# Optimization experiments

Hardware: AMD Instinct MI355X
Metric: run time of the kernel (lower is better)

The kernel has to match this reference:

```python
import jax, jax.numpy as jnp
import numpy as np
from jax import lax

# Fixed dims from MSSMamba defaults
B_, L_, DM = 2, 8192, 256
NH, HP, NS = 4, 64, 8          # nheads, headdim, d_state
DIN = NH * HP                  # d_inner = 256
DPROJ = 2 * DIN + 2 * NS + NH  # 532


def setup_inputs() -> dict:
    key = jax.random.key(0)
    ks = jax.random.split(key, 16)
    f = lambda k, s, sc=1.0: jax.random.normal(k, s, jnp.float32) * sc
    inp = {
        'x_H': f(ks[0], (B_, L_, DM)),
        'x_V': f(ks[1], (B_, L_, DM)),
        'W_in_H': f(ks[2], (DM, 2 * DPROJ), 0.05),
        'W_in_V': f(ks[3], (DM, 2 * DPROJ), 0.05),
        'W_out_HF': f(ks[4], (DIN, DM), 0.05),
        'W_out_HB': f(ks[5], (DIN, DM), 0.05),
        'W_out_VF': f(ks[6], (DIN, DM), 0.05),
        'W_out_VB': f(ks[7], (DIN, DM), 0.05),
        'W_out': f(ks[8], (4 * DM, DM), 0.05),
    }
    for i, nm in enumerate(['HF', 'HB', 'VF', 'VB']):
        kd = jax.random.fold_in(ks[9], i)
        ka = jax.random.fold_in(ks[10], i)
        inp['dt_bias_' + nm] = f(kd, (NH,), 0.1)
        inp['A_log_' + nm] = jnp.log(jax.random.uniform(ka, (NH,), jnp.float32, 1.0, 16.0))
        inp['D_' + nm] = jnp.ones((NH,), jnp.float32)
    # per-batch permutation mapping vertical position -> horizontal position
    inp['v2h'] = jax.vmap(lambda k: jax.random.permutation(k, L_))(
        jax.random.split(ks[11], B_)).astype(jnp.int32)
    return inp


def _scan_dir(zxbcdt, dt_bias, A_log, D):
    # zxbcdt: [b, l, DPROJ] -> Mamba2-style selective scan, ngroups=1
    z = zxbcdt[..., :DIN].reshape(B_, L_, NH, HP)
    xBC = jax.nn.silu(zxbcdt[..., DIN:DIN + DIN + 2 * NS])
    x = xBC[..., :DIN].reshape(B_, L_, NH, HP)
    Bm = xBC[..., DIN:DIN + NS]      # [b, l, n]
    Cm = xBC[..., DIN + NS:]         # [b, l, n]
    dt = jax.nn.softplus(zxbcdt[..., -NH:] + dt_bias)  # [b, l, h]
    A = -jnp.exp(A_log)              # [h]
    dA = jnp.exp(dt * A)             # [b, l, h]
    dBx = jnp.einsum('blh,bln,blhp->blhpn', dt, Bm, x)  # [b,l,h,p,n]

    def step(state, inp):
        dA_t, dBx_t, C_t = inp
        state = dA_t[..., None, None] * state + dBx_t   # [b,h,p,n]
        y_t = jnp.einsum('bhpn,bn->bhp', state, C_t)
        return state, y_t

    init = jnp.zeros((B_, NH, HP, NS), dt.dtype)
    _, ys = lax.scan(step, init, (jnp.moveaxis(dA, 1, 0),
                                  jnp.moveaxis(dBx, 1, 0),
                                  jnp.moveaxis(Cm, 1, 0)))
    y = jnp.moveaxis(ys, 0, 1) + D[None, None, :, None] * x  # skip D*x
    y = y * jax.nn.silu(z)                                   # gate
    return y.reshape(B_, L_, DIN)


def reference(x_H, x_V, W_in_H, W_in_V,
              dt_bias_HF, dt_bias_HB, dt_bias_VF, dt_bias_VB,
              A_log_HF, A_log_HB, A_log_VF, A_log_VB,
              D_HF, D_HB, D_VF, D_VB,
              W_out_HF, W_out_HB, W_out_VF, W_out_VB,
              W_out, v2h):
    zx_HF, zx_HB = jnp.split(x_H @ W_in_H, 2, axis=-1)
    zx_VF, zx_VB = jnp.split(x_V @ W_in_V, 2, axis=-1)
    # note: source applies out_proj_HB to the HF branch (kept faithful)
    y_HF = _scan_dir(zx_HF, dt_bias_HF, A_log_HF, D_HF) @ W_out_HB
    y_HB = _scan_dir(zx_HB[:, ::-1], dt_bias_HB, A_log_HB, D_HB)[:, ::-1] @ W_out_HF
    y_VF = _scan_dir(zx_VF, dt_bias_VF, A_log_VF, D_VF) @ W_out_VB
    y_VB = _scan_dir(zx_VB[:, ::-1], dt_bias_VB, A_log_VB, D_VB)[:, ::-1] @ W_out_VF
    # remap vertical-ordered outputs to horizontal ordering (scatter by v2h)
    bidx = jnp.arange(B_)[:, None]
    y_VF = jnp.zeros_like(y_VF).at[bidx, v2h].set(y_VF)
    y_VB = jnp.zeros_like(y_VB).at[bidx, v2h].set(y_VB)
    cat = jnp.concatenate([y_HF, y_HB, y_VF, y_VB], axis=-1)  # [b, l, 4*d_model]
    return jax.nn.silu(cat) @ W_out
```

## Files before the change

### kernel.cpp

```cpp
#include <hip/hip_runtime.h>
#include <hip/hip_bf16.h>

#define B_N 2
#define L_N 8192
#define ROWS 16384
#define CHUNK 64
#define NCHUNK 128
#define GRP 16
#define NGRP 8
#define NPAD 1152

typedef __bf16 bf16x8 __attribute__((ext_vector_type(8)));
typedef float f32x4 __attribute__((ext_vector_type(4)));

__device__ __forceinline__ float siluf(float v) {
  return v * __builtin_amdgcn_rcpf(1.f + __expf(-v));
}
__device__ __forceinline__ float softplusf_(float v) {
  return fmaxf(v, 0.f) + log1pf(__expf(-fabsf(v)));
}
__device__ __forceinline__ unsigned short f2bf(float v) {
  union { __bf16 b; unsigned short u; } x;
  x.b = (__bf16)v;
  return x.u;
}
__device__ __forceinline__ float bf2f(unsigned short u) {
  union { unsigned u; float f; } x; x.u = ((unsigned)u) << 16;
  return x.f;
}

__device__ __forceinline__ void gload_lds16(const unsigned short* g, unsigned short* l) {
  __builtin_amdgcn_global_load_lds(
      (const __attribute__((address_space(1))) unsigned int*)g,
      (__attribute__((address_space(3))) unsigned int*)l, 16, 0, 0);
}

struct P4 { const float* p[4]; };
struct ScanConsts {
  const float* dt_bias[4];
  const float* A_log[4];
  const float* D[4];
};

__global__ __launch_bounds__(256) void k_prep(
    const float* __restrict__ xH, const float* __restrict__ xV,
    const float* __restrict__ WH, const float* __restrict__ WV,
    P4 ws, const float* __restrict__ W_out, const int* __restrict__ v2h, ScanConsts sc,
    unsigned short* __restrict__ xbf, float* __restrict__ dtv_arr, float* __restrict__ dA_arr,
    unsigned short* __restrict__ Wt_in, unsigned short* __restrict__ Wt_dirs,
    unsigned short* __restrict__ Wt_fin, int* __restrict__ inv) {
  __shared__ float xs[32][257];
  __shared__ float Wsm[8][260];
  int bid = blockIdx.x;
  int tid = threadIdx.x;
  if (bid < 1024) {
    const int mat = bid >> 9;
    const float* x = mat ? xV : xH;
    const float* W = mat ? WV : WH;
    const int r0 = (bid & 511) * 32;
    for (int i = tid; i < 2048; i += 256) {
      int c = i >> 8, k = i & 255;
      int sl = c >> 2, h = c & 3;
      Wsm[c][k] = W[(long)k * 1064 + sl * 532 + 528 + h];
    }
    for (int i = tid; i < 32 * 64; i += 256) {
      int rl = i >> 6, kq = (i & 63) * 4;
      float4 v = *(const float4*)(x + (long)(r0 + rl) * 256 + kq);
      xs[rl][kq + 0] = v.x; xs[rl][kq + 1] = v.y; xs[rl][kq + 2] = v.z; xs[rl][kq + 3] = v.w;
    }
    __syncthreads();
    for (int i = tid; i < 32 * 64; i += 256) {
      int rl = i >> 6, kq = (i & 63) * 4;
      ushort4 o;
      o.x = f2bf(xs[rl][kq + 0]);
      o.y = f2bf(xs[rl][kq + 1]);
      o.z = f2bf(xs[rl][kq + 2]);
      o.w = f2bf(xs[rl][kq + 3]);
      *(ushort4*)(xbf + (size_t)mat * ROWS * 256 + (long)(r0 + rl) * 256 + kq) = o;
    }
    const int rl = tid >> 3, c = tid & 7;
    float s = 0.f;
    #pragma unroll 8
    for (int k = 0; k < 256; ++k) s = fmaf(xs[rl][k], Wsm[c][k], s);
    const int sl = c >> 2, h = c & 3;
    const int dir = mat * 2 + sl;
    float dtv = softplusf_(s + sc.dt_bias[dir][h]);
    float dAv = __expf(dtv * (-__expf(sc.A_log[dir][h])));
    long o = ((long)dir * 4 + h) * ROWS + (r0 + rl);
    dtv_arr[o] = dtv;
    dA_arr[o] = dAv;
  } else if (bid < 3328) {
    int i = (bid - 1024) * 256 + tid;
    int z = i / (NPAD * 256);
    int rem = i - z * (NPAD * 256);
    int n = rem >> 8, k = rem & 255;
    const float* W = z ? WV : WH;
    int sl = n >= 544;
    int cc = n - (sl ? 544 : 0);
    float v = (cc < 532) ? W[(long)k * 1064 + sl * 532 + cc] : 0.f;
    Wt_in[i] = f2bf(v);
  } else if (bid < 4352) {
    int i = (bid - 3328) * 256 + tid;
    int d = i >> 16;
    int rem = i & 65535;
    int n = rem >> 8, k = rem & 255;
    Wt_dirs[i] = f2bf(ws.p[d][(long)k * 256 + n]);
  } else if (bid < 5376) {
    int i = (bid - 4352) * 256 + tid;
    int n = i >> 10, k = i & 1023;
    Wt_fin[i] = f2bf(W_out[(long)k * 256 + n]);
  } else {
    int m = (bid - 5376) * 256 + tid;
    if (m < ROWS) {
      int b = m >> 13;
      inv[b * L_N + v2h[m]] = m;
    }
  }
}

struct EpiIn {
  unsigned short* zraw;
  unsigned short* xraw;
  unsigned short* bc;
};

__global__ __launch_bounds__(256) void k_gemm_in(
    const unsigned short* __restrict__ Abase, const unsigned short* __restrict__ Btbase,
    EpiIn ep) {
  __shared__ unsigned short smem[24576];
  const int tid = threadIdx.x;
  const int lane = tid & 63;
  const int wid = tid >> 6;
  const int wm = wid & 1, wn = wid >> 1;
  const int q = lane >> 4, r = lane & 15;
  const int hbid = blockIdx.x;
  const int xcd = hbid & 7;
  const int j = hbid >> 3;
  const int m0 = (xcd * 16 + (j & 15)) * 128;
  const int n0 = ((j >> 4) % 9) * 128;
  const int z = j / 144;
  const unsigned short* A = Abase + (long)z * ROWS * 256;
  const unsigned short* Bt = Btbase + (long)z * NPAD * 256;

  int s_row[2], s_ch[2];
  #pragma unroll
  for (int i = 0; i < 2; ++i) {
    int idx = i * 256 + tid;
    s_row[i] = idx >> 2;
    s_ch[i] = (idx & 3) ^ ((s_row[i] >> 1) & 3);
  }

  auto stage = [&](int ti) {
    const int slot = ti % 3;
    const int kt = ti * 32;
    #pragma unroll
    for (int i = 0; i < 2; ++i) {
      gload_lds16(A + (long)(m0 + s_row[i]) * 256 + kt + s_ch[i] * 8,
                  smem + (size_t)slot * 4096 + (size_t)(i * 256 + wid * 64) * 8);
      gload_lds16(Bt + (long)(n0 + s_row[i]) * 256 + kt + s_ch[i] * 8,
                  smem + 12288 + (size_t)slot * 4096 + (size_t)(i * 256 + wid * 64) * 8);
    }
  };

  f32x4 acc[4][4] = {};
  const int swr = (r >> 1) & 3;

  stage(0);
  stage(1);

  #pragma unroll
  for (int i = 0; i < 8; ++i) {
    if (i < 7) asm volatile("s_waitcnt vmcnt(4)" ::: "memory");
    else       asm volatile("s_waitcnt vmcnt(0)" ::: "memory");
    __builtin_amdgcn_s_barrier();
    __builtin_amdgcn_sched_barrier(0);
    if (i + 2 < 8) stage(i + 2);
    const int slot = i % 3;
    bf16x8 af[4], bfr[4];
    #pragma unroll
    for (int mi = 0; mi < 4; ++mi)
      af[mi] = *(const bf16x8*)&smem[(size_t)slot * 4096 +
                                     ((wm * 64 + mi * 16 + r) * 4 + (q ^ swr)) * 8];
    #pragma unroll
    for (int ni = 0; ni < 4; ++ni)
      bfr[ni] = *(const bf16x8*)&smem[12288 + (size_t)slot * 4096 +
                                      ((wn * 64 + ni * 16 + r) * 4 + (q ^ swr)) * 8];
    __builtin_amdgcn_s_setprio(1);
    #pragma unroll
    for (int mi = 0; mi < 4; ++mi)
      #pragma unroll
      for (int ni = 0; ni < 4; ++ni)
        acc[mi][ni] = __builtin_amdgcn_mfma_f32_16x16x32_bf16(af[mi], bfr[ni], acc[mi][ni], 0, 0, 0);
    __builtin_amdgcn_s_setprio(0);
  }
  __syncthreads();

  unsigned short* tr = smem + wid * (16 * 72);
  #pragma unroll
  for (int mi = 0; mi < 4; ++mi) {
    #pragma unroll
    for (int ni = 0; ni < 4; ++ni)
      #pragma unroll
      for (int j2 = 0; j2 < 4; ++j2)
        tr[(q * 4 + j2) * 72 + ni * 16 + r] = f2bf(acc[mi][ni][j2]);
    asm volatile("s_waitcnt lgkmcnt(0)" ::: "memory");
    #pragma unroll
    for (int pass = 0; pass < 2; ++pass) {
      int rl = pass * 8 + (lane >> 3);
      int c8 = (lane & 7) * 8;
      bf16x8 v = *(const bf16x8*)&tr[rl * 72 + c8];
      int row = m0 + wm * 64 + mi * 16 + rl;
      int col = n0 + wn * 64 + c8;
      int sl = col >= 544;
      int cc = col - (sl ? 544 : 0);
      if (cc < 528) {
        int dir = z * 2 + sl;
        if (cc < 256)
          *(bf16x8*)(ep.zraw + ((long)dir * ROWS + row) * 256 + cc) = v;
        else if (cc < 512)
          *(bf16x8*)(ep.xraw + ((long)dir * ROWS + row) * 256 + cc - 256) = v;
        else
          *(bf16x8*)(ep.bc + ((long)dir * ROWS + row) * 16 + cc - 512) = v;
      }
    }
    asm volatile("s_waitcnt lgkmcnt(0)" ::: "memory");
  }
}

__global__ __launch_bounds__(512) void k_fuse(
    const unsigned short* __restrict__ ybf,
    const unsigned short* __restrict__ Wt_dirs,
    const unsigned short* __restrict__ Wt_fin,
    const int* __restrict__ inv,
    float* __restrict__ out) {
  __shared__ unsigned short smf[47616];
  unsigned short* Ab = smf;
  unsigned short* Bb = smf + 6144;
  unsigned short* Tl = smf + 30720;
  float* Ttmp = (float*)(smf + 30720);
  const int tid = threadIdx.x;
  const int lane = tid & 63;
  const int wid = tid >> 6;
  const int wm = wid & 1, wn = wid >> 1;
  const int q = lane >> 4, r = lane & 15;
  const int r0 = blockIdx.x * 64;
  const int swr = (r >> 1) & 3;

  const int a_row = tid >> 2;
  const int a_ch = (tid & 3) ^ ((a_row >> 1) & 3);
  const long a_offH = (long)(r0 + a_row) * 256 + a_ch * 8;
  long a_offV = 0;
  if (tid < 256) a_offV = (long)inv[r0 + a_row] * 256 + a_ch * 8;
  int b_row[2], b_ch[2];
  #pragma unroll
  for (int rnd = 0; rnd < 2; ++rnd) {
    int idx = rnd * 512 + tid;
    b_row[rnd] = idx >> 2;
    b_ch[rnd] = (idx & 3) ^ ((b_row[rnd] >> 1) & 3);
  }

  auto stageT = [&](int g) {
    const int seg = g >> 3, ti = g & 7, kt = ti * 32;
    const int dl = seg >> 1;
    const int slot = g % 3;
    if ((seg & 1) == 0) {
      const long aoff = (dl >= 2) ? a_offV : a_offH;
      if (tid < 256)
        gload_lds16(ybf + (long)dl * ROWS * 256 + aoff + kt,
                    Ab + (size_t)slot * 2048 + (size_t)(wid * 64) * 8);
      #pragma unroll
      for (int rnd = 0; rnd < 2; ++rnd)
        gload_lds16(Wt_dirs + (long)dl * 65536 + (long)b_row[rnd] * 256 + kt + b_ch[rnd] * 8,
                    Bb + (size_t)slot * 8192 + (size_t)(rnd * 512 + wid * 64) * 8);
    } else {
      #pragma unroll
      for (int rnd = 0; rnd < 2; ++rnd)
        gload_lds16(Wt_fin + (long)b_row[rnd] * 1024 + dl * 256 + kt + b_ch[rnd] * 8,
                    Bb + (size_t)slot * 8192 + (size_t)(rnd * 512 + wid * 64) * 8);
    }
  };

  f32x4 acc_o[2][4] = {};

  stageT(0);
  stageT(1);

  #pragma unroll
  for (int d = 0; d < 4; ++d) {
    f32x4 acc_t[2][4] = {};
    #pragma unroll
    for (int i = 0; i < 8; ++i) {
      const int g = d * 16 + i;
      asm volatile("s_waitcnt vmcnt(2)" ::: "memory");
      __builtin_amdgcn_s_barrier();
      __builtin_amdgcn_sched_barrier(0);
      stageT(g + 2);
      const int slot = g % 3;
      bf16x8 af[2], bfr[4];
      #pragma unroll
      for (int mi = 0; mi < 2; ++mi)
        af[mi] = *(const bf16x8*)&Ab[(size_t)slot * 2048 +
                                     ((wm * 32 + mi * 16 + r) * 4 + (q ^ swr)) * 8];
      #pragma unroll
      for (int ni = 0; ni < 4; ++ni)
        bfr[ni] = *(const bf16x8*)&Bb[(size_t)slot * 8192 +
                                      ((wn * 64 + ni * 16 + r) * 4 + (q ^ swr)) * 8];
      __builtin_amdgcn_s_setprio(1);
      #pragma unroll
      for (int mi = 0; mi < 2; ++mi)
        #pragma unroll
        for (int ni = 0; ni < 4; ++ni)
          acc_t[mi][ni] = __builtin_amdgcn_mfma_f32_16x16x32_bf16(af[mi], bfr[ni], acc_t[mi][ni], 0, 0, 0);
      __builtin_amdgcn_s_setprio(0);
    }
    #pragma unroll
    for (int mi = 0; mi < 2; ++mi)
      #pragma unroll
      for (int ni = 0; ni < 4; ++ni)
        #pragma unroll
        for (int jj = 0; jj < 4; ++jj)
          Tl[(wm * 32 + mi * 16 + q * 4 + jj) * 264 + wn * 64 + ni * 16 + r] =
              f2bf(siluf(acc_t[mi][ni][jj]));
    asm volatile("s_waitcnt lgkmcnt(0)" ::: "memory");
    #pragma unroll
    for (int i = 0; i < 8; ++i) {
      const int g = d * 16 + 8 + i;
      if (g < 63) asm volatile("s_waitcnt vmcnt(2)" ::: "memory");
      else        asm volatile("s_waitcnt vmcnt(0)" ::: "memory");
      __builtin_amdgcn_s_barrier();
      __builtin_amdgcn_sched_barrier(0);
      if (g + 2 < 64) stageT(g + 2);
      const int slot = g % 3;
      const int kt = i * 32;
      bf16x8 af[2], bfr[4];
      #pragma unroll
      for (int mi = 0; mi < 2; ++mi)
        af[mi] = *(const bf16x8*)&Tl[(wm * 32 + mi * 16 + r) * 264 + kt + q * 8];
      #pragma unroll
      for (int ni = 0; ni < 4; ++ni)
        bfr[ni] = *(const bf16x8*)&Bb[(size_t)slot * 8192 +
                                      ((wn * 64 + ni * 16 + r) * 4 + (q ^ swr)) * 8];
      __builtin_amdgcn_s_setprio(1);
      #pragma unroll
      for (int mi = 0; mi < 2; ++mi)
        #pragma unroll
        for (int ni = 0; ni < 4; ++ni)
          acc_o[mi][ni] = __builtin_amdgcn_mfma_f32_16x16x32_bf16(af[mi], bfr[ni], acc_o[mi][ni], 0, 0, 0);
      __builtin_amdgcn_s_setprio(0);
    }
  }

  __syncthreads();
  #pragma unroll
  for (int h = 0; h < 2; ++h) {
    if (wm == h) {
      #pragma unroll
      for (int mi = 0; mi < 2; ++mi)
        #pragma unroll
        for (int ni = 0; ni < 4; ++ni)
          #pragma unroll
          for (int jj = 0; jj < 4; ++jj)
            Ttmp[(mi * 16 + q * 4 + jj) * 260 + wn * 64 + ni * 16 + r] = acc_o[mi][ni][jj];
    }
    __syncthreads();
    #pragma unroll
    for (int pass = 0; pass < 4; ++pass) {
      int id = pass * 512 + tid;
      int row = id >> 6, c4 = (id & 63) * 4;
      float4 v = *(const float4*)&Ttmp[row * 260 + c4];
      *(float4*)(out + (long)(r0 + h * 32 + row) * 256 + c4) = v;
    }
    if (h == 0) __syncthreads();
  }
}

struct ScanP {
  const unsigned short* xraw;
  const unsigned short* zraw;
  const unsigned short* bc;
  const float* dtv;
  const float* dA;
  const float* D[4];
};

__global__ __launch_bounds__(512) void k_scan1(ScanP sp, float* __restrict__ S,
                                               float* __restrict__ P) {
  __shared__ __align__(16) float Bst[8][CHUNK][8];
  __shared__ float dAs[8][CHUNK];
  const int tid = threadIdx.x;
  const int p = tid & 63;
  const int w = tid >> 6;
  const int c = blockIdx.x;
  const int d = blockIdx.y;
  const int bh = w;
  const int b = bh >> 2, h = bh & 3;
  const int rev = d & 1;
  const int t0 = c * CHUNK;
  {
    const int t = t0 + p;
    const int l = rev ? (L_N - 1 - t) : t;
    const int row = (b << 13) + l;
    uint4 bv = *(const uint4*)(sp.bc + ((long)d * ROWS + row) * 16);
    const unsigned short* bu = (const unsigned short*)&bv;
    float dtvv = sp.dtv[((long)d * 4 + h) * ROWS + row];
    dAs[w][p] = sp.dA[((long)d * 4 + h) * ROWS + row];
    #pragma unroll
    for (int n = 0; n < 8; ++n) Bst[w][p][n] = siluf(bf2f(bu[n])) * dtvv;
  }
  __syncthreads();

  float st[8] = {0, 0, 0, 0, 0, 0, 0, 0};
  float cumdA = 1.f;
  const int l0 = rev ? (L_N - 1 - t0) : t0;
  const unsigned short* xp = sp.xraw + ((long)d * ROWS + (b << 13) + l0) * 256 + h * 64 + p;
  const long stp = rev ? -256L : 256L;

  unsigned short xa[4], xb[4];
  #pragma unroll
  for (int j = 0; j < 4; ++j) xa[j] = xp[(long)j * stp];
  #pragma unroll
  for (int g = 0; g < CHUNK / 4; ++g) {
    if (g < CHUNK / 4 - 1) {
      #pragma unroll
      for (int j = 0; j < 4; ++j) xb[j] = xp[(long)((g + 1) * 4 + j) * stp];
    }
    #pragma unroll
    for (int j = 0; j < 4; ++j) {
      int s = g * 4 + j;
      float x = siluf(bf2f(xa[j]));
      float dA = dAs[w][s];
      f32x4 B0 = *(const f32x4*)&Bst[w][s][0];
      f32x4 B1 = *(const f32x4*)&Bst[w][s][4];
      cumdA *= dA;
      st[0] = fmaf(dA, st[0], x * B0[0]);
      st[1] = fmaf(dA, st[1], x * B0[1]);
      st[2] = fmaf(dA, st[2], x * B0[2]);
      st[3] = fmaf(dA, st[3], x * B0[3]);
      st[4] = fmaf(dA, st[4], x * B1[0]);
      st[5] = fmaf(dA, st[5], x * B1[1]);
      st[6] = fmaf(dA, st[6], x * B1[2]);
      st[7] = fmaf(dA, st[7], x * B1[3]);
    }
    #pragma unroll
    for (int j = 0; j < 4; ++j) xa[j] = xb[j];
  }
  float* Sp = S + ((((long)d * NCHUNK + c) * 8 + bh) * 64 + p) * 8;
  #pragma unroll
  for (int n = 0; n < 8; ++n) Sp[n] = st[n];
  if (p == 0) P[((long)d * NCHUNK + c) * 8 + bh] = cumdA;
}

__global__ __launch_bounds__(512) void k_scan2a(const float* __restrict__ S,
                                                const float* __restrict__ P,
                                                float* __restrict__ carry_loc,
                                                float* __restrict__ Sg,
                                                float* __restrict__ Pg) {
  __shared__ float Pl[GRP];
  const int tid = threadIdx.x;
  const int gid = blockIdx.x;
  const int g = gid & (NGRP - 1);
  const int dbh = gid >> 3;
  const int d = dbh >> 3, bh = dbh & 7;
  if (tid < GRP) Pl[tid] = P[((long)d * NCHUNK + g * GRP + tid) * 8 + bh];
  __syncthreads();
  float cy = 0.f;
  #pragma unroll
  for (int i = 0; i < GRP; ++i) {
    const int c = g * GRP + i;
    carry_loc[(((long)d * NCHUNK + c) * 8 + bh) * 512 + tid] = cy;
    const float Sv = S[(((long)d * NCHUNK + c) * 8 + bh) * 512 + tid];
    cy = fmaf(Pl[i], cy, Sv);
  }
  Sg[(((long)d * NGRP + g) * 8 + bh) * 512 + tid] = cy;
  if (tid == 0) {
    float pp = 1.f;
    #pragma unroll
    for (int i = 0; i < GRP; ++i) pp *= Pl[i];
    Pg[((long)d * NGRP + g) * 8 + bh] = pp;
  }
}

__global__ __launch_bounds__(512) void k_scan2b(const float* __restrict__ Sg,
                                                const float* __restrict__ Pg,
                                                float* __restrict__ gcarry) {
  __shared__ float Pgl[NGRP];
  const int tid = threadIdx.x;
  const int dbh = blockIdx.x;
  const int d = dbh >> 3, bh = dbh & 7;
  if (tid < NGRP) Pgl[tid] = Pg[((long)d * NGRP + tid) * 8 + bh];
  __syncthreads();
  float cy = 0.f;
  #pragma unroll
  for (int g = 0; g < NGRP; ++g) {
    gcarry[(((long)d * NGRP + g) * 8 + bh) * 512 + tid] = cy;
    const float Sv = Sg[(((long)d * NGRP + g) * 8 + bh) * 512 + tid];
    cy = fmaf(Pgl[g], cy, Sv);
  }
}

__global__ __launch_bounds__(512) void k_scan3(ScanP sp,
                                               const float* __restrict__ carry_loc,
                                               const float* __restrict__ gcarry,
                                               const float* __restrict__ Pc,
                                               unsigned short* __restrict__ ybf) {
  __shared__ __align__(16) float Bst[8][CHUNK][8];
  __shared__ __align__(16) float Cst[8][CHUNK][8];
  __shared__ float dAs[8][CHUNK];
  __shared__ float Pgr[8][GRP];
  const int tid = threadIdx.x;
  const int p = tid & 63;
  const int w = tid >> 6;
  const int c = blockIdx.x;
  const int d = blockIdx.y;
  const int bh = w;
  const int b = bh >> 2, h = bh & 3;
  const int rev = d & 1;
  const float Dv = sp.D[d][h];
  const int t0 = c * CHUNK;
  const int grp = c >> 4, ii = c & 15;
  if (p < ii) Pgr[w][p] = Pc[((long)d * NCHUNK + grp * GRP + p) * 8 + bh];
  {
    const int t = t0 + p;
    const int l = rev ? (L_N - 1 - t) : t;
    const int row = (b << 13) + l;
    const unsigned short* bp = sp.bc + ((long)d * ROWS + row) * 16;
    uint4 bv = *(const uint4*)bp;
    uint4 cv = *(const uint4*)(bp + 8);
    const unsigned short* bu = (const unsigned short*)&bv;
    const unsigned short* cu = (const unsigned short*)&cv;
    float dtvv = sp.dtv[((long)d * 4 + h) * ROWS + row];
    dAs[w][p] = sp.dA[((long)d * 4 + h) * ROWS + row];
    #pragma unroll
    for (int n = 0; n < 8; ++n) Bst[w][p][n] = siluf(bf2f(bu[n])) * dtvv;
    #pragma unroll
    for (int n = 0; n < 8; ++n) Cst[w][p][n] = siluf(bf2f(cu[n]));
  }
  __syncthreads();

  float pref = 1.f;
  for (int k = 0; k < ii; ++k) pref *= Pgr[w][k];
  float st[8];
  {
    const float* clp = carry_loc + ((((long)d * NCHUNK + c) * 8 + bh) * 64 + p) * 8;
    const float* gcp = gcarry + ((((long)d * NGRP + grp) * 8 + bh) * 64 + p) * 8;
    #pragma unroll
    for (int n = 0; n < 8; ++n) st[n] = fmaf(pref, gcp[n], clp[n]);
  }

  const int l0 = rev ? (L_N - 1 - t0) : t0;
  const long base = (long)(b << 13) + l0;
  const unsigned short* xp = sp.xraw + ((long)d * ROWS + base) * 256 + h * 64 + p;
  const unsigned short* zp = sp.zraw + ((long)d * ROWS + base) * 256 + h * 64 + p;
  unsigned short* yp = ybf + ((long)d * ROWS + base) * 256 + h * 64 + p;
  const long stp = rev ? -256L : 256L;

  unsigned short xa[4], xb[4], za[4], zb[4];
  #pragma unroll
  for (int j = 0; j < 4; ++j) { xa[j] = xp[(long)j * stp]; za[j] = zp[(long)j * stp]; }
  #pragma unroll
  for (int g = 0; g < CHUNK / 4; ++g) {
    if (g < CHUNK / 4 - 1) {
      #pragma unroll
      for (int j = 0; j < 4; ++j) {
        xb[j] = xp[(long)((g + 1) * 4 + j) * stp];
        zb[j] = zp[(long)((g + 1) * 4 + j) * stp];
      }
    }
    #pragma unroll
    for (int j = 0; j < 4; ++j) {
      int s = g * 4 + j;
      float x = siluf(bf2f(xa[j]));
      float zv = siluf(bf2f(za[j]));
      float dA = dAs[w][s];
      f32x4 B0 = *(const f32x4*)&Bst[w][s][0];
      f32x4 B1 = *(const f32x4*)&Bst[w][s][4];
      f32x4 C0 = *(const f32x4*)&Cst[w][s][0];
      f32x4 C1 = *(const f32x4*)&Cst[w][s][4];
      st[0] = fmaf(dA, st[0], x * B0[0]);
      st[1] = fmaf(dA, st[1], x * B0[1]);
      st[2] = fmaf(dA, st[2], x * B0[2]);
      st[3] = fmaf(dA, st[3], x * B0[3]);
      st[4] = fmaf(dA, st[4], x * B1[0]);
      st[5] = fmaf(dA, st[5], x * B1[1]);
      st[6] = fmaf(dA, st[6], x * B1[2]);
      st[7] = fmaf(dA, st[7], x * B1[3]);
      float y01 = fmaf(st[1], C0[1], st[0] * C0[0]);
      float y23 = fmaf(st[3], C0[3], st[2] * C0[2]);
      float y45 = fmaf(st[5], C1[1], st[4] * C1[0]);
      float y67 = fmaf(st[7], C1[3], st[6] * C1[2]);
      float y = (y01 + y23) + (y45 + y67);
      y = fmaf(Dv, x, y) * zv;
      yp[(long)s * stp] = f2bf(y);
    }
    #pragma unroll
    for (int j = 0; j < 4; ++j) { xa[j] = xb[j]; za[j] = zb[j]; }
  }
}

extern "C" void kernel_launch(void* const* d_in, const int* in_sizes, int n_in,
                              void* d_out, int out_size, void* d_ws, size_t ws_size,
                              hipStream_t stream) {
  const float* x_H = (const float*)d_in[0];
  const float* x_V = (const float*)d_in[1];
  const float* W_in_H = (const float*)d_in[2];
  const float* W_in_V = (const float*)d_in[3];
  const float* W_out_HF = (const float*)d_in[4];
  const float* W_out_HB = (const float*)d_in[5];
  const float* W_out_VF = (const float*)d_in[6];
  const float* W_out_VB = (const float*)d_in[7];
  const float* W_out = (const float*)d_in[8];
  const float* dt_bias_HF = (const float*)d_in[9];
  const float* A_log_HF = (const float*)d_in[10];
  const float* D_HF = (const float*)d_in[11];
  const float* dt_bias_HB = (const float*)d_in[12];
  const float* A_log_HB = (const float*)d_in[13];
  const float* D_HB = (const float*)d_in[14];
  const float* dt_bias_VF = (const float*)d_in[15];
  const float* A_log_VF = (const float*)d_in[16];
  const float* D_VF = (const float*)d_in[17];
  const float* dt_bias_VB = (const float*)d_in[18];
  const float* A_log_VB = (const float*)d_in[19];
  const float* D_VB = (const float*)d_in[20];
  const int* v2h = (const int*)d_in[21];

  char* ws = (char*)d_ws;
  size_t off = 0;
  auto alloc = [&](size_t bytes) {
    void* pp = ws + off;
    off = (off + bytes + 255) & ~(size_t)255;
    return pp;
  };
  unsigned short* xbf = (unsigned short*)alloc((size_t)2 * ROWS * 256 * 2);
  unsigned short* Wt_in = (unsigned short*)alloc((size_t)2 * NPAD * 256 * 2);
  unsigned short* Wt_dirs = (unsigned short*)alloc((size_t)4 * 65536 * 2);
  unsigned short* Wt_fin = (unsigned short*)alloc((size_t)256 * 1024 * 2);
  unsigned short* zraw = (unsigned short*)alloc((size_t)4 * ROWS * 256 * 2);
  unsigned short* xraw = (unsigned short*)alloc((size_t)4 * ROWS * 256 * 2);
  unsigned short* bc = (unsigned short*)alloc((size_t)4 * ROWS * 16 * 2);
  float* dtv_arr = (float*)alloc((size_t)16 * ROWS * 4);
  float* dA_arr = (float*)alloc((size_t)16 * ROWS * 4);
  unsigned short* ybf = (unsigned short*)alloc((size_t)4 * ROWS * 256 * 2);
  float* S = (float*)alloc((size_t)4 * NCHUNK * 8 * 512 * 4);
  float* P = (float*)alloc((size_t)4 * NCHUNK * 8 * 4);
  float* carry_loc = (float*)alloc((size_t)4 * NCHUNK * 8 * 512 * 4);
  float* Sg = (float*)alloc((size_t)4 * NGRP * 8 * 512 * 4);
  float* Pg = (float*)alloc((size_t)4 * NGRP * 8 * 4);
  float* gcarry = (float*)alloc((size_t)4 * NGRP * 8 * 512 * 4);
  int* inv = (int*)alloc((size_t)ROWS * 4);

  ScanConsts sc;
  sc.dt_bias[0] = dt_bias_HF; sc.dt_bias[1] = dt_bias_HB;
  sc.dt_bias[2] = dt_bias_VF; sc.dt_bias[3] = dt_bias_VB;
  sc.A_log[0] = A_log_HF; sc.A_log[1] = A_log_HB;
  sc.A_log[2] = A_log_VF; sc.A_log[3] = A_log_VB;
  sc.D[0] = D_HF; sc.D[1] = D_HB; sc.D[2] = D_VF; sc.D[3] = D_VB;

  P4 wdirs;
  wdirs.p[0] = W_out_HB; wdirs.p[1] = W_out_HF; wdirs.p[2] = W_out_VB; wdirs.p[3] = W_out_VF;

  k_prep<<<5440, 256, 0, stream>>>(x_H, x_V, W_in_H, W_in_V, wdirs, W_out, v2h, sc,
                                   xbf, dtv_arr, dA_arr, Wt_in, Wt_dirs, Wt_fin, inv);

  EpiIn ep; ep.zraw = zraw; ep.xraw = xraw; ep.bc = bc;

  k_gemm_in<<<2304, 256, 0, stream>>>(xbf, Wt_in, ep);

  ScanP sp;
  sp.xraw = xraw; sp.zraw = zraw; sp.bc = bc; sp.dtv = dtv_arr; sp.dA = dA_arr;
  sp.D[0] = D_HF; sp.D[1] = D_HB; sp.D[2] = D_VF; sp.D[3] = D_VB;

  k_scan1<<<dim3(NCHUNK, 4), 512, 0, stream>>>(sp, S, P);
  k_scan2a<<<32 * NGRP, 512, 0, stream>>>(S, P, carry_loc, Sg, Pg);
  k_scan2b<<<32, 512, 0, stream>>>(Sg, Pg, gcarry);
  k_scan3<<<dim3(NCHUNK, 4), 512, 0, stream>>>(sp, carry_loc, gcarry, P, ybf);

  k_fuse<<<256, 512, 0, stream>>>(ybf, Wt_dirs, Wt_fin, inv, (float*)d_out);

  (void)in_sizes; (void)n_in; (void)out_size; (void)ws_size;
}
```

Before: 237.0 us.

## Remap chunked scan to one wave per (dir,batch,chunk) with 4 channels per lane

The scan kernels move from 512-thread blocks (one wave per batch-head) to 64-thread blocks where each lane handles 4 adjacent channels, so the whole 256-wide row is read and written with vector ushort4 accesses. B, C, dt and dA are staged once per chunk for all heads, and the dt multiply moves from B to x. The state and carry arrays and the scan2a/2b indexing are relaid out to match. Each lane now carries 32 state registers, which raises register pressure and leaves only 1024 small blocks, with fewer lanes working on the sequential recurrence at a time.

```diff
diff --git a/kernel.cpp b/kernel.cpp
--- a/kernel.cpp
+++ b/kernel.cpp
@@ -383,17 +383,16 @@
   const float* D[4];
 };
 
-__global__ __launch_bounds__(512) void k_scan1(ScanP sp, float* __restrict__ S,
-                                               float* __restrict__ P) {
-  __shared__ __align__(16) float Bst[8][CHUNK][8];
-  __shared__ float dAs[8][CHUNK];
-  const int tid = threadIdx.x;
-  const int p = tid & 63;
-  const int w = tid >> 6;
+
+__global__ __launch_bounds__(64) void k_scan1(ScanP sp, float* __restrict__ S,
+                                              float* __restrict__ P) {
+  __shared__ __align__(16) float Bst[CHUNK][8];
+  __shared__ float dAs[CHUNK][4];
+  __shared__ float dts[CHUNK][4];
+  const int p = threadIdx.x;
   const int c = blockIdx.x;
-  const int d = blockIdx.y;
-  const int bh = w;
-  const int b = bh >> 2, h = bh & 3;
+  const int db = blockIdx.y;
+  const int d = db >> 1, b = db & 1;
   const int rev = d & 1;
   const int t0 = c * CHUNK;
   {
@@ -402,52 +401,60 @@
     const int row = (b << 13) + l;
     uint4 bv = *(const uint4*)(sp.bc + ((long)d * ROWS + row) * 16);
     const unsigned short* bu = (const unsigned short*)&bv;
-    float dtvv = sp.dtv[((long)d * 4 + h) * ROWS + row];
-    dAs[w][p] = sp.dA[((long)d * 4 + h) * ROWS + row];
-    #pragma unroll
-    for (int n = 0; n < 8; ++n) Bst[w][p][n] = siluf(bf2f(bu[n])) * dtvv;
+    #pragma unroll
+    for (int n = 0; n < 8; ++n) Bst[p][n] = siluf(bf2f(bu[n]));
+    #pragma unroll
+    for (int hh = 0; hh < 4; ++hh) {
+      dts[p][hh] = sp.dtv[((long)d * 4 + hh) * ROWS + row];
+      dAs[p][hh] = sp.dA[((long)d * 4 + hh) * ROWS + row];
+    }
   }
   __syncthreads();
 
-  float st[8] = {0, 0, 0, 0, 0, 0, 0, 0};
+  const int h = p >> 4;
+  float st[4][8] = {};
   float cumdA = 1.f;
   const int l0 = rev ? (L_N - 1 - t0) : t0;
-  const unsigned short* xp = sp.xraw + ((long)d * ROWS + (b << 13) + l0) * 256 + h * 64 + p;
+  const unsigned short* xp = sp.xraw + ((long)d * ROWS + (b << 13) + l0) * 256 + 4 * p;
   const long stp = rev ? -256L : 256L;
 
-  unsigned short xa[4], xb[4];
-  #pragma unroll
-  for (int j = 0; j < 4; ++j) xa[j] = xp[(long)j * stp];
+  ushort4 xa[4], xb[4];
+  #pragma unroll
+  for (int j = 0; j < 4; ++j) xa[j] = *(const ushort4*)(xp + (long)j * stp);
   #pragma unroll
   for (int g = 0; g < CHUNK / 4; ++g) {
     if (g < CHUNK / 4 - 1) {
       #pragma unroll
-      for (int j = 0; j < 4; ++j) xb[j] = xp[(long)((g + 1) * 4 + j) * stp];
+      for (int j = 0; j < 4; ++j)
+        xb[j] = *(const ushort4*)(xp + (long)((g + 1) * 4 + j) * stp);
     }
     #pragma unroll
     for (int j = 0; j < 4; ++j) {
-      int s = g * 4 + j;
-      float x = siluf(bf2f(xa[j]));
-      float dA = dAs[w][s];
-      f32x4 B0 = *(const f32x4*)&Bst[w][s][0];
-      f32x4 B1 = *(const f32x4*)&Bst[w][s][4];
+      const int s = g * 4 + j;
+      const float dA = dAs[s][h];
+      const float dt = dts[s][h];
       cumdA *= dA;
-      st[0] = fmaf(dA, st[0], x * B0[0]);
-      st[1] = fmaf(dA, st[1], x * B0[1]);
-      st[2] = fmaf(dA, st[2], x * B0[2]);
-      st[3] = fmaf(dA, st[3], x * B0[3]);
-      st[4] = fmaf(dA, st[4], x * B1[0]);
-      st[5] = fmaf(dA, st[5], x * B1[1]);
-      st[6] = fmaf(dA, st[6], x * B1[2]);
-      st[7] = fmaf(dA, st[7], x * B1[3]);
+      const unsigned short* xu = (const unsigned short*)&xa[j];
+      #pragma unroll
+      for (int cc = 0; cc < 4; ++cc) {
+        float xd = siluf(bf2f(xu[cc])) * dt;
+        #pragma unroll
+        for (int n = 0; n < 8; ++n)
+          st[cc][n] = fmaf(dA, st[cc][n], xd * Bst[s][n]);
+      }
     }
     #pragma unroll
     for (int j = 0; j < 4; ++j) xa[j] = xb[j];
   }
-  float* Sp = S + ((((long)d * NCHUNK + c) * 8 + bh) * 64 + p) * 8;
-  #pragma unroll
-  for (int n = 0; n < 8; ++n) Sp[n] = st[n];
-  if (p == 0) P[((long)d * NCHUNK + c) * 8 + bh] = cumdA;
+  float* Sp = S + ((long)(d * NCHUNK + c) * 2 + b) * 2048 + p * 32;
+  #pragma unroll
+  for (int cc = 0; cc < 4; ++cc) {
+    f32x4 v0 = {st[cc][0], st[cc][1], st[cc][2], st[cc][3]};
+    f32x4 v1 = {st[cc][4], st[cc][5], st[cc][6], st[cc][7]};
+    *(f32x4*)(Sp + cc * 8) = v0;
+    *(f32x4*)(Sp + cc * 8 + 4) = v1;
+  }
+  if ((p & 15) == 0) P[((long)(d * NCHUNK + c) * 2 + b) * 4 + h] = cumdA;
 }
 
 __global__ __launch_bounds__(512) void k_scan2a(const float* __restrict__ S,
@@ -458,25 +465,29 @@
   __shared__ float Pl[GRP];
   const int tid = threadIdx.x;
   const int gid = blockIdx.x;
-  const int g = gid & (NGRP - 1);
-  const int dbh = gid >> 3;
-  const int d = dbh >> 3, bh = dbh & 7;
-  if (tid < GRP) Pl[tid] = P[((long)d * NCHUNK + g * GRP + tid) * 8 + bh];
+  const int d = gid >> 6;
+  const int b = (gid >> 5) & 1;
+  const int g = (gid >> 2) & 7;
+  const int q = gid & 3;
+  if (tid < GRP)
+    Pl[tid] = P[((long)(d * NCHUNK + g * GRP + tid) * 2 + b) * 4 + q];
   __syncthreads();
+  const int e = q * 512 + tid;
   float cy = 0.f;
   #pragma unroll
   for (int i = 0; i < GRP; ++i) {
     const int c = g * GRP + i;
-    carry_loc[(((long)d * NCHUNK + c) * 8 + bh) * 512 + tid] = cy;
-    const float Sv = S[(((long)d * NCHUNK + c) * 8 + bh) * 512 + tid];
+    const long base = ((long)(d * NCHUNK + c) * 2 + b) * 2048;
+    carry_loc[base + e] = cy;
+    const float Sv = S[base + e];
     cy = fmaf(Pl[i], cy, Sv);
   }
-  Sg[(((long)d * NGRP + g) * 8 + bh) * 512 + tid] = cy;
+  Sg[((long)(d * NGRP + g) * 2 + b) * 2048 + e] = cy;
   if (tid == 0) {
     float pp = 1.f;
     #pragma unroll
     for (int i = 0; i < GRP; ++i) pp *= Pl[i];
-    Pg[((long)d * NGRP + g) * 8 + bh] = pp;
+    Pg[((long)(d * NGRP + g) * 2 + b) * 4 + q] = pp;
   }
 }
 
@@ -485,40 +496,45 @@
                                                 float* __restrict__ gcarry) {
   __shared__ float Pgl[NGRP];
   const int tid = threadIdx.x;
-  const int dbh = blockIdx.x;
-  const int d = dbh >> 3, bh = dbh & 7;
-  if (tid < NGRP) Pgl[tid] = Pg[((long)d * NGRP + tid) * 8 + bh];
+  const int gid = blockIdx.x;
+  const int d = gid >> 3;
+  const int b = (gid >> 2) & 1;
+  const int q = gid & 3;
+  if (tid < NGRP)
+    Pgl[tid] = Pg[((long)(d * NGRP + tid) * 2 + b) * 4 + q];
   __syncthreads();
+  const int e = q * 512 + tid;
   float cy = 0.f;
   #pragma unroll
   for (int g = 0; g < NGRP; ++g) {
-    gcarry[(((long)d * NGRP + g) * 8 + bh) * 512 + tid] = cy;
-    const float Sv = Sg[(((long)d * NGRP + g) * 8 + bh) * 512 + tid];
+    const long base = ((long)(d * NGRP + g) * 2 + b) * 2048;
+    gcarry[base + e] = cy;
+    const float Sv = Sg[base + e];
     cy = fmaf(Pgl[g], cy, Sv);
   }
 }
 
-__global__ __launch_bounds__(512) void k_scan3(ScanP sp,
-                                               const float* __restrict__ carry_loc,
-                                               const float* __restrict__ gcarry,
-                                               const float* __restrict__ Pc,
-                                               unsigned short* __restrict__ ybf) {
-  __shared__ __align__(16) float Bst[8][CHUNK][8];
-  __shared__ __align__(16) float Cst[8][CHUNK][8];
-  __shared__ float dAs[8][CHUNK];
-  __shared__ float Pgr[8][GRP];
-  const int tid = threadIdx.x;
-  const int p = tid & 63;
-  const int w = tid >> 6;
+__global__ __launch_bounds__(64) void k_scan3(ScanP sp,
+                                              const float* __restrict__ carry_loc,
+                                              const float* __restrict__ gcarry,
+                                              const float* __restrict__ Pc,
+                                              unsigned short* __restrict__ ybf) {
+  __shared__ __align__(16) float Bst[CHUNK][8];
+  __shared__ __align__(16) float Cst[CHUNK][8];
+  __shared__ float dAs[CHUNK][4];
+  __shared__ float dts[CHUNK][4];
+  __shared__ float Pgr[GRP][4];
+  const int p = threadIdx.x;
   const int c = blockIdx.x;
-  const int d = blockIdx.y;
-  const int bh = w;
-  const int b = bh >> 2, h = bh & 3;
+  const int db = blockIdx.y;
+  const int d = db >> 1, b = db & 1;
   const int rev = d & 1;
-  const float Dv = sp.D[d][h];
   const int t0 = c * CHUNK;
   const int grp = c >> 4, ii = c & 15;
-  if (p < ii) Pgr[w][p] = Pc[((long)d * NCHUNK + grp * GRP + p) * 8 + bh];
+  if (p < 64) {
+    int k = p >> 2, hh = p & 3;
+    Pgr[k][hh] = Pc[((long)(d * NCHUNK + grp * GRP + k) * 2 + b) * 4 + hh];
+  }
   {
     const int t = t0 + p;
     const int l = rev ? (L_N - 1 - t) : t;
@@ -528,69 +544,81 @@
     uint4 cv = *(const uint4*)(bp + 8);
     const unsigned short* bu = (const unsigned short*)&bv;
     const unsigned short* cu = (const unsigned short*)&cv;
-    float dtvv = sp.dtv[((long)d * 4 + h) * ROWS + row];
-    dAs[w][p] = sp.dA[((long)d * 4 + h) * ROWS + row];
-    #pragma unroll
-    for (int n = 0; n < 8; ++n) Bst[w][p][n] = siluf(bf2f(bu[n])) * dtvv;
-    #pragma unroll
-    for (int n = 0; n < 8; ++n) Cst[w][p][n] = siluf(bf2f(cu[n]));
+    #pragma unroll
+    for (int n = 0; n < 8; ++n) Bst[p][n] = siluf(bf2f(bu[n]));
+    #pragma unroll
+    for (int n = 0; n < 8; ++n) Cst[p][n] = siluf(bf2f(cu[n]));
+    #pragma unroll
+    for (int hh = 0; hh < 4; ++hh) {
+      dts[p][hh] = sp.dtv[((long)d * 4 + hh) * ROWS + row];
+      dAs[p][hh] = sp.dA[((long)d * 4 + hh) * ROWS + row];
+    }
   }
   __syncthreads();
 
+  const int h = p >> 4;
+  const float Dv = sp.D[d][h];
   float pref = 1.f;
-  for (int k = 0; k < ii; ++k) pref *= Pgr[w][k];
-  float st[8];
+  for (int k = 0; k < ii; ++k) pref *= Pgr[k][h];
+  float st[4][8];
   {
-    const float* clp = carry_loc + ((((long)d * NCHUNK + c) * 8 + bh) * 64 + p) * 8;
-    const float* gcp = gcarry + ((((long)d * NGRP + grp) * 8 + bh) * 64 + p) * 8;
-    #pragma unroll
-    for (int n = 0; n < 8; ++n) st[n] = fmaf(pref, gcp[n], clp[n]);
+    const float* clp = carry_loc + ((long)(d * NCHUNK + c) * 2 + b) * 2048 + p * 32;
+    const float* gcp = gcarry + ((long)(d * NGRP + grp) * 2 + b) * 2048 + p * 32;
+    #pragma unroll
+    for (int cc = 0; cc < 4; ++cc)
+      #pragma unroll
+      for (int n = 0; n < 8; ++n)
+        st[cc][n] = fmaf(pref, gcp[cc * 8 + n], clp[cc * 8 + n]);
   }
 
   const int l0 = rev ? (L_N - 1 - t0) : t0;
   const long base = (long)(b << 13) + l0;
-  const unsigned short* xp = sp.xraw + ((long)d * ROWS + base) * 256 + h * 64 + p;
-  const unsigned short* zp = sp.zraw + ((long)d * ROWS + base) * 256 + h * 64 + p;
-  unsigned short* yp = ybf + ((long)d * ROWS + base) * 256 + h * 64 + p;
+  const unsigned short* xp = sp.xraw + ((long)d * ROWS + base) * 256 + 4 * p;
+  const unsigned short* zp = sp.zraw + ((long)d * ROWS + base) * 256 + 4 * p;
+  unsigned short* yp = ybf + ((long)d * ROWS + base) * 256 + 4 * p;
   const long stp = rev ? -256L : 256L;
 
-  unsigned short xa[4], xb[4], za[4], zb[4];
-  #pragma unroll
-  for (int j = 0; j < 4; ++j) { xa[j] = xp[(long)j * stp]; za[j] = zp[(long)j * stp]; }
+  ushort4 xa[4], xb[4], za[4], zb[4];
+  #pragma unroll
+  for (int j = 0; j < 4; ++j) {
+    xa[j] = *(const ushort4*)(xp + (long)j * stp);
+    za[j] = *(const ushort4*)(zp + (long)j * stp);
+  }
   #pragma unroll
   for (int g = 0; g < CHUNK / 4; ++g) {
     if (g < CHUNK / 4 - 1) {
       #pragma unroll
       for (int j = 0; j < 4; ++j) {
-        xb[j] = xp[(long)((g + 1) * 4 + j) * stp];
-        zb[j] = zp[(long)((g + 1) * 4 + j) * stp];
+        xb[j] = *(const ushort4*)(xp + (long)((g + 1) * 4 + j) * stp);
+        zb[j] = *(const ushort4*)(zp + (long)((g + 1) * 4 + j) * stp);
       }
     }
     #pragma unroll
     for (int j = 0; j < 4; ++j) {
-      int s = g * 4 + j;
-      float x = siluf(bf2f(xa[j]));
-      float zv = siluf(bf2f(za[j]));
-      float dA = dAs[w][s];
-      f32x4 B0 = *(const f32x4*)&Bst[w][s][0];
-      f32x4 B1 = *(const f32x4*)&Bst[w][s][4];
-      f32x4 C0 = *(const f32x4*)&Cst[w][s][0];
-      f32x4 C1 = *(const f32x4*)&Cst[w][s][4];
-      st[0] = fmaf(dA, st[0], x * B0[0]);
-      st[1] = fmaf(dA, st[1], x * B0[1]);
-      st[2] = fmaf(dA, st[2], x * B0[2]);
-      st[3] = fmaf(dA, st[3], x * B0[3]);
-      st[4] = fmaf(dA, st[4], x * B1[0]);
-      st[5] = fmaf(dA, st[5], x * B1[1]);
-      st[6] = fmaf(dA, st[6], x * B1[2]);
-      st[7] = fmaf(dA, st[7], x * B1[3]);
-      float y01 = fmaf(st[1], C0[1], st[0] * C0[0]);
-      float y23 = fmaf(st[3], C0[3], st[2] * C0[2]);
-      float y45 = fmaf(st[5], C1[1], st[4] * C1[0]);
-      float y67 = fmaf(st[7], C1[3], st[6] * C1[2]);
-      float y = (y01 + y23) + (y45 + y67);
-      y = fmaf(Dv, x, y) * zv;
-      yp[(long)s * stp] = f2bf(y);
+      const int s = g * 4 + j;
+      const float dA = dAs[s][h];
+      const float dt = dts[s][h];
+      const unsigned short* xu = (const unsigned short*)&xa[j];
+      const unsigned short* zu = (const unsigned short*)&za[j];
+      ushort4 o;
+      unsigned short* ou = (unsigned short*)&o;
+      #pragma unroll
+      for (int cc = 0; cc < 4; ++cc) {
+        float xv = siluf(bf2f(xu[cc]));
+        float zv = siluf(bf2f(zu[cc]));
+        float xd = xv * dt;
+        #pragma unroll
+        for (int n = 0; n < 8; ++n)
+          st[cc][n] = fmaf(dA, st[cc][n], xd * Bst[s][n]);
+        float y01 = fmaf(st[cc][1], Cst[s][1], st[cc][0] * Cst[s][0]);
+        float y23 = fmaf(st[cc][3], Cst[s][3], st[cc][2] * Cst[s][2]);
+        float y45 = fmaf(st[cc][5], Cst[s][5], st[cc][4] * Cst[s][4]);
+        float y67 = fmaf(st[cc][7], Cst[s][7], st[cc][6] * Cst[s][6]);
+        float y = (y01 + y23) + (y45 + y67);
+        y = fmaf(Dv, xv, y) * zv;
+        ou[cc] = f2bf(y);
+      }
+      *(ushort4*)(yp + (long)s * stp) = o;
     }
     #pragma unroll
     for (int j = 0; j < 4; ++j) { xa[j] = xb[j]; za[j] = zb[j]; }
@@ -640,12 +668,12 @@
   float* dtv_arr = (float*)alloc((size_t)16 * ROWS * 4);
   float* dA_arr = (float*)alloc((size_t)16 * ROWS * 4);
   unsigned short* ybf = (unsigned short*)alloc((size_t)4 * ROWS * 256 * 2);
-  float* S = (float*)alloc((size_t)4 * NCHUNK * 8 * 512 * 4);
-  float* P = (float*)alloc((size_t)4 * NCHUNK * 8 * 4);
-  float* carry_loc = (float*)alloc((size_t)4 * NCHUNK * 8 * 512 * 4);
-  float* Sg = (float*)alloc((size_t)4 * NGRP * 8 * 512 * 4);
-  float* Pg = (float*)alloc((size_t)4 * NGRP * 8 * 4);
-  float* gcarry = (float*)alloc((size_t)4 * NGRP * 8 * 512 * 4);
+  float* S = (float*)alloc((size_t)4 * NCHUNK * 2 * 2048 * 4);
+  float* P = (float*)alloc((size_t)4 * NCHUNK * 2 * 4 * 4);
+  float* carry_loc = (float*)alloc((size_t)4 * NCHUNK * 2 * 2048 * 4);
+  float* Sg = (float*)alloc((size_t)4 * NGRP * 2 * 2048 * 4);
+  float* Pg = (float*)alloc((size_t)4 * NGRP * 2 * 4 * 4);
+  float* gcarry = (float*)alloc((size_t)4 * NGRP * 2 * 2048 * 4);
   int* inv = (int*)alloc((size_t)ROWS * 4);
 
   ScanConsts sc;
@@ -669,10 +697,10 @@
   sp.xraw = xraw; sp.zraw = zraw; sp.bc = bc; sp.dtv = dtv_arr; sp.dA = dA_arr;
   sp.D[0] = D_HF; sp.D[1] = D_HB; sp.D[2] = D_VF; sp.D[3] = D_VB;
 
-  k_scan1<<<dim3(NCHUNK, 4), 512, 0, stream>>>(sp, S, P);
-  k_scan2a<<<32 * NGRP, 512, 0, stream>>>(S, P, carry_loc, Sg, Pg);
+  k_scan1<<<dim3(NCHUNK, 8), 64, 0, stream>>>(sp, S, P);
+  k_scan2a<<<256, 512, 0, stream>>>(S, P, carry_loc, Sg, Pg);
   k_scan2b<<<32, 512, 0, stream>>>(Sg, Pg, gcarry);
-  k_scan3<<<dim3(NCHUNK, 4), 512, 0, stream>>>(sp, carry_loc, gcarry, P, ybf);
+  k_scan3<<<dim3(NCHUNK, 8), 64, 0, stream>>>(sp, carry_loc, gcarry, P, ybf);
 
   k_fuse<<<256, 512, 0, stream>>>(ybf, Wt_dirs, Wt_fin, inv, (float*)d_out);
 
```

After: 429.4 us. 1.81x slower.
